# Performance work log

Measured on AMD Instinct MI355X. Metric: run time of the kernel, lower is better.

The kernel has to match this reference:

```python
import jax, jax.numpy as jnp
import numpy as np

NUM_HEADS = 32
HEAD_DIM = 512
EPS = 1e-12  # torch F.normalize eps


def setup_inputs() -> dict:
    key = jax.random.key(0)
    k1, k2, k3, k4, k5 = jax.random.split(key, 5)
    B, C, H, W = 32, 256, 64, 64
    return {
        "X": jax.random.normal(k1, (B, C, H, W), dtype=jnp.float32),
        "qkv_w": jax.random.normal(k2, (3 * HEAD_DIM, C), dtype=jnp.float32) * 0.02,
        "qkv_b": jax.random.normal(k3, (3 * HEAD_DIM,), dtype=jnp.float32) * 0.02,
        "proj_w": jax.random.normal(k4, (C, HEAD_DIM), dtype=jnp.float32) * 0.02,
        "proj_b": jax.random.normal(k5, (C,), dtype=jnp.float32) * 0.02,
    }


def _l2norm_axis1(x):
    # torch F.normalize(x, dim=1): x / max(||x||_2, eps)
    n = jnp.sqrt(jnp.sum(x * x, axis=1, keepdims=True))
    return x / jnp.maximum(n, EPS)


def reference(X, qkv_w, qkv_b, proj_w, proj_b):
    B, C, H, W = X.shape
    # 1x1 conv == channel matmul: [B,3*hd,H,W]
    qkv = jnp.einsum('bchw,oc->bohw', X, qkv_w) + qkv_b[None, :, None, None]
    # reshape to (B, 3, num_heads, head_dim, L) where L = H*W // num_heads
    qkv = qkv.reshape(B, 3, NUM_HEADS, HEAD_DIM, -1)
    q, k, v = qkv[:, 0], qkv[:, 1], qkv[:, 2]  # [B, nh, hd, L]
    # normalize across the num_heads axis (dim=1), as in the original code
    q = _l2norm_axis1(q)
    k = _l2norm_axis1(k)
    # attn = q^T @ k : [B, nh, L, L]
    attn = jnp.einsum('bhdl,bhdm->bhlm', q, k)
    attn = jax.nn.softmax(attn, axis=-1)
    # output = v @ attn^T : [B, nh, hd, L]
    out = jnp.einsum('bhdm,bhlm->bhdl', v, attn)
    out = out.reshape(B, HEAD_DIM, H, W)
    # proj 1x1 conv back to C channels
    out = jnp.einsum('bdhw,cd->bchw', out, proj_w) + proj_b[None, :, None, None]
    return out
```

## Files before the change

### kernel.cpp

```cpp
#include <hip/hip_runtime.h>
#include <stdint.h>


typedef float     f32x4   __attribute__((ext_vector_type(4)));
typedef short     bf16x8  __attribute__((ext_vector_type(8)));
typedef float     floatx4 __attribute__((ext_vector_type(4)));
typedef uint16_t  ushortx8 __attribute__((ext_vector_type(8)));
typedef uint16_t  ushortx4 __attribute__((ext_vector_type(4)));

#define DEVI static __device__ __forceinline__

DEVI float bf2f(uint16_t u) { union { uint32_t i; float f; } x; x.i = ((uint32_t)u) << 16; return x.f; }
DEVI uint16_t f2bf(float f) {
  union { float f; uint32_t i; } x; x.f = f;
  uint32_t r = x.i + 0x7fff + ((x.i >> 16) & 1);
  return (uint16_t)(r >> 16);
}

DEVI void gload16(const void* g, void* l) {
  __builtin_amdgcn_global_load_lds((const __attribute__((address_space(1))) void*)g,
                                   (__attribute__((address_space(3))) void*)l, 16, 0, 0);
}

DEVI float redmax16(float v) {
  v = fmaxf(v, __shfl_xor(v, 1)); v = fmaxf(v, __shfl_xor(v, 2));
  v = fmaxf(v, __shfl_xor(v, 4)); v = fmaxf(v, __shfl_xor(v, 8));
  return v;
}
DEVI float redsum16(float v) {
  v += __shfl_xor(v, 1); v += __shfl_xor(v, 2);
  v += __shfl_xor(v, 4); v += __shfl_xor(v, 8);
  return v;
}

__global__ __launch_bounds__(256) void k_transpose_x(const float* __restrict__ X,
                                                     uint16_t* __restrict__ Xt) {
  __shared__ float tile[64][65];
  int t = threadIdx.x;
  int st = blockIdx.x, ct = blockIdx.y, b = blockIdx.z;
  int row = t >> 2, cq = t & 3;
  const float* src = X + ((size_t)(b * 256 + ct * 64 + row)) * 4096 + st * 64 + cq * 16;
#pragma unroll
  for (int k = 0; k < 4; ++k) {
    floatx4 v = *(const floatx4*)(src + k * 4);
    tile[row][cq * 16 + k * 4 + 0] = v[0];
    tile[row][cq * 16 + k * 4 + 1] = v[1];
    tile[row][cq * 16 + k * 4 + 2] = v[2];
    tile[row][cq * 16 + k * 4 + 3] = v[3];
  }
  __syncthreads();
  int srow = t >> 2, oq = t & 3;
  ushortx8 o0, o1;
#pragma unroll
  for (int k = 0; k < 8; ++k) o0[k] = f2bf(tile[oq * 16 + k][srow]);
#pragma unroll
  for (int k = 0; k < 8; ++k) o1[k] = f2bf(tile[oq * 16 + 8 + k][srow]);
  uint16_t* dst = Xt + ((size_t)(b * 4096 + st * 64 + srow)) * 256 + ct * 64 + oq * 16;
  *(ushortx8*)dst = o0;
  *(ushortx8*)(dst + 8) = o1;
}

__global__ __launch_bounds__(256) void k_cvt_bf16(const float* __restrict__ src,
                                                  uint16_t* __restrict__ dst, int n) {
  int i = (blockIdx.x * 256 + threadIdx.x) * 4;
  if (i >= n) return;
  floatx4 v = *(const floatx4*)(src + i);
  ushortx4 o;
  o[0] = f2bf(v[0]); o[1] = f2bf(v[1]); o[2] = f2bf(v[2]); o[3] = f2bf(v[3]);
  *(ushortx4*)(dst + i) = o;
}

__global__ __launch_bounds__(256) void k_qkv_gemm(const uint16_t* __restrict__ W,
                                                  const uint16_t* __restrict__ Xt,
                                                  const float* __restrict__ bias_g,
                                                  uint16_t* __restrict__ qkv) {
  __shared__ __align__(16) union {
    uint16_t ab[2][128 * 64];
    uint16_t c[128 * 136];
  } sm;
  uint16_t* As = sm.ab[0];
  uint16_t* Bs = sm.ab[1];
  int t = threadIdx.x, lane = t & 63, wave = t >> 6;
  int ot = blockIdx.x, st = blockIdx.y, b = blockIdx.z;
  int wr = wave >> 1, wc = wave & 1;
  f32x4 acc[4][4] = {};
  int srow = lane >> 3;
  int sc_us = ((((lane & 7) * 16) ^ ((srow & 7) << 4)) >> 1);
  const uint16_t* Ag = W + (size_t)(ot * 128 + wave * 8 + srow) * 256;
  const uint16_t* Bg = Xt + ((size_t)(b * 4096 + st * 128 + wave * 8 + srow)) * 256;

  for (int kc = 0; kc < 4; ++kc) {
    __syncthreads();
#pragma unroll
    for (int c = 0; c < 4; ++c) {
      gload16(Ag + (size_t)(c * 32) * 256 + kc * 64 + sc_us, &As[(c * 32 + wave * 8) * 64]);
      gload16(Bg + (size_t)(c * 32) * 256 + kc * 64 + sc_us, &Bs[(c * 32 + wave * 8) * 64]);
    }
    __syncthreads();
#pragma unroll
    for (int kk = 0; kk < 2; ++kk) {
      bf16x8 a[4], bw[4];
#pragma unroll
      for (int i = 0; i < 4; ++i) {
        int r = wr * 64 + i * 16 + (lane & 15);
        a[i] = *(const bf16x8*)&As[r * 64 + ((kk * 32 + (lane >> 4) * 8) ^ ((r & 7) << 3))];
      }
#pragma unroll
      for (int j = 0; j < 4; ++j) {
        int r = wc * 64 + j * 16 + (lane & 15);
        bw[j] = *(const bf16x8*)&Bs[r * 64 + ((kk * 32 + (lane >> 4) * 8) ^ ((r & 7) << 3))];
      }
#pragma unroll
      for (int i = 0; i < 4; ++i)
#pragma unroll
        for (int j = 0; j < 4; ++j)
          acc[i][j] = __builtin_amdgcn_mfma_f32_16x16x32_bf16(a[i], bw[j], acc[i][j], 0, 0, 0);
    }
  }
  int o0 = ot * 128 + wr * 64;
  float bv[4][4];
#pragma unroll
  for (int i = 0; i < 4; ++i)
#pragma unroll
    for (int r = 0; r < 4; ++r) bv[i][r] = bias_g[o0 + i * 16 + (lane >> 4) * 4 + r];
  __syncthreads();
#pragma unroll
  for (int i = 0; i < 4; ++i)
#pragma unroll
    for (int j = 0; j < 4; ++j)
#pragma unroll
      for (int r = 0; r < 4; ++r) {
        int ol = wr * 64 + i * 16 + (lane >> 4) * 4 + r;
        int sl = wc * 64 + j * 16 + (lane & 15);
        sm.c[ol * 136 + sl] = f2bf(acc[i][j][r] + bv[i][r]);
      }
  __syncthreads();
  uint16_t* outb = qkv + ((size_t)b * 1536 + ot * 128) * 4096 + st * 128;
  int rrow = t >> 4, rcol = (t & 15) * 8;
#pragma unroll
  for (int p = 0; p < 8; ++p) {
    int row = p * 16 + rrow;
    ushortx8 v = *(ushortx8*)&sm.c[row * 136 + rcol];
    *(ushortx8*)(outb + (size_t)row * 4096 + rcol) = v;
  }
}

__global__ __launch_bounds__(256) void k_scales(const uint16_t* __restrict__ qkv,
                                                float* __restrict__ scaleB) {
  int t = threadIdx.x;
  int sc = blockIdx.x, g = blockIdx.y, b = blockIdx.z;
  const uint16_t* base = qkv + ((size_t)(b * 1536 + g * 512)) * 4096;
  float* sb = scaleB + (size_t)b * 524288 + (size_t)g * 65536;
  int c16 = t >> 4, so = t & 15;
  int s = sc * 128 + so * 8;
  float ss[8] = {};
  for (int h = 0; h < 32; ++h) {
    ushortx8 v = *(const ushortx8*)(base + ((size_t)(h * 16 + c16)) * 4096 + s);
#pragma unroll
    for (int j = 0; j < 8; ++j) { float f = bf2f(v[j]); ss[j] += f * f; }
  }
  floatx4 o0, o1;
#pragma unroll
  for (int j = 0; j < 4; ++j) o0[j] = 1.0f / fmaxf(sqrtf(ss[j]), 1e-12f);
#pragma unroll
  for (int j = 0; j < 4; ++j) o1[j] = 1.0f / fmaxf(sqrtf(ss[4 + j]), 1e-12f);
  *(floatx4*)(sb + c16 * 4096 + s) = o0;
  *(floatx4*)(sb + c16 * 4096 + s + 4) = o1;
}

__global__ __launch_bounds__(512, 4) void k_attn(const uint16_t* __restrict__ qkv,
                                                 const float* __restrict__ scaleB,
                                                 uint16_t* OtAll) {
  __shared__ __align__(16) uint16_t smemA[16384];
  __shared__ __align__(16) uint16_t Pb[16384];
  __shared__ float rsum[128];
  int t = threadIdx.x, lane = t & 63, w = t >> 6;
  int h = blockIdx.x, b = blockIdx.y;
  const uint16_t* qg = qkv + ((size_t)(b * 1536) + h * 16) * 4096;
  const uint16_t* kg = qkv + ((size_t)(b * 1536) + 512 + h * 16) * 4096;
  const float* sq = scaleB + (size_t)b * 524288;
  const float* sk = sq + 65536;
  uint16_t* QT = smemA;
  uint16_t* KT = smemA + 8192;

  int sl = t & 127;
  int dd8a = t >> 7;

  f32x4 accs[8] = {};
  for (int kc = 0; kc < 8; ++kc) {
    __syncthreads();
#pragma unroll
    for (int kq = 0; kq < 2; ++kq) {
      int dd8 = dd8a + kq * 4;
      int c16 = kc * 2 + (dd8 >> 2);
      int s0 = (dd8 & 3) * 8;
      const uint16_t* qrow = qg + (size_t)c16 * 4096 + sl;
      const uint16_t* krow = kg + (size_t)c16 * 4096 + sl;
      const float* sqr = sq + c16 * 4096 + sl;
      const float* skr = sk + c16 * 4096 + sl;
      ushortx8 oq, ok;
#pragma unroll
      for (int j = 0; j < 8; ++j) {
        int soff = (s0 + j) * 128;
        oq[j] = f2bf(bf2f(qrow[soff]) * sqr[soff]);
        ok[j] = f2bf(bf2f(krow[soff]) * skr[soff]);
      }
      int lidx = sl * 64 + ((dd8 * 8) ^ ((sl & 7) << 3));
      *(ushortx8*)&QT[lidx] = oq;
      *(ushortx8*)&KT[lidx] = ok;
    }
    __syncthreads();
#pragma unroll
    for (int kk = 0; kk < 2; ++kk) {
      int ra = w * 16 + (lane & 15);
      bf16x8 aq = *(const bf16x8*)&QT[ra * 64 + ((kk * 32 + (lane >> 4) * 8) ^ ((ra & 7) << 3))];
#pragma unroll
      for (int mf = 0; mf < 8; ++mf) {
        int rm = mf * 16 + (lane & 15);
        bf16x8 bk = *(const bf16x8*)&KT[rm * 64 + ((kk * 32 + (lane >> 4) * 8) ^ ((rm & 7) << 3))];
        accs[mf] = __builtin_amdgcn_mfma_f32_16x16x32_bf16(aq, bk, accs[mf], 0, 0, 0);
      }
    }
  }

#pragma unroll
  for (int r = 0; r < 4; ++r) {
    float mx = accs[0][r];
#pragma unroll
    for (int mf = 1; mf < 8; ++mf) mx = fmaxf(mx, accs[mf][r]);
    mx = redmax16(mx);
    float sum = 0.f;
#pragma unroll
    for (int mf = 0; mf < 8; ++mf) {
      float e = __expf(accs[mf][r] - mx);
      accs[mf][r] = e;
      sum += e;
    }
    sum = redsum16(sum);
    int l = w * 16 + (lane >> 4) * 4 + r;
    if ((lane & 15) == 0) rsum[l] = 1.0f / sum;
#pragma unroll
    for (int mf = 0; mf < 8; ++mf) {
      int m = mf * 16 + (lane & 15);
      Pb[l * 128 + (m ^ ((l & 7) << 3))] = f2bf(accs[mf][r]);
    }
  }
  __syncthreads();

  const uint16_t* vg = qkv + ((size_t)(b * 1536) + 1024 + h * 16) * 4096;
  uint16_t* OtT = OtAll + (size_t)b * 6291456;
  int vrow = lane >> 2;
  int vcol_us = ((((lane & 3) * 16) ^ ((vrow & 3) << 4)) >> 1);

#pragma unroll
  for (int lc = 0; lc < 2; ++lc) {
    f32x4 acco[4][4] = {};
    for (int mc = 0; mc < 4; ++mc) {
      __syncthreads();
#pragma unroll
      for (int c = 0; c < 4; ++c) {
        int d = w * 64 + c * 16 + vrow;
        gload16(vg + (size_t)(d >> 5) * 4096 + (d & 31) * 128 + mc * 32 + vcol_us,
                &smemA[(w * 64 + c * 16) * 32]);
      }
      __syncthreads();
      bf16x8 bp[4];
#pragma unroll
      for (int lf = 0; lf < 4; ++lf) {
        int l = lc * 64 + lf * 16 + (lane & 15);
        bp[lf] = *(const bf16x8*)&Pb[l * 128 + ((mc * 32 + (lane >> 4) * 8) ^ ((l & 7) << 3))];
      }
#pragma unroll
      for (int df = 0; df < 4; ++df) {
        int rv = w * 64 + df * 16 + (lane & 15);
        bf16x8 av = *(const bf16x8*)&smemA[rv * 32 + (((lane >> 4) * 8) ^ ((rv & 3) << 3))];
#pragma unroll
        for (int lf = 0; lf < 4; ++lf)
          acco[df][lf] = __builtin_amdgcn_mfma_f32_16x16x32_bf16(av, bp[lf], acco[df][lf], 0, 0, 0);
      }
    }
    float scl[4];
#pragma unroll
    for (int lf = 0; lf < 4; ++lf) scl[lf] = rsum[lc * 64 + lf * 16 + (lane & 15)];
#pragma unroll
    for (int df = 0; df < 4; ++df)
#pragma unroll
      for (int r = 0; r < 4; ++r) {
        int d = w * 64 + df * 16 + (lane >> 4) * 4 + r;
        uint16_t* orow = OtT + ((size_t)(h * 16 + (d >> 5))) * 4096 + (d & 31) * 128;
#pragma unroll
        for (int lf = 0; lf < 4; ++lf) {
          int l = lc * 64 + lf * 16 + (lane & 15);
          orow[l] = f2bf(acco[df][lf][r] * scl[lf]);
        }
      }
  }
}

__global__ __launch_bounds__(256) void k_proj_gemm(const uint16_t* __restrict__ Wp,
                                                   const uint16_t* __restrict__ OtAll,
                                                   const float* __restrict__ bias_g,
                                                   float* __restrict__ outp) {
  __shared__ __align__(16) uint16_t As[128 * 64];
  __shared__ __align__(16) uint16_t Bs[128 * 64];
  int t = threadIdx.x, lane = t & 63, wave = t >> 6;
  int st = blockIdx.x, ct = blockIdx.y, b = blockIdx.z;
  int wr = wave >> 1, wc = wave & 1;
  f32x4 acc[4][4] = {};
  int srow = lane >> 3;
  int sc_us = ((((lane & 7) * 16) ^ ((srow & 7) << 4)) >> 1);
  const uint16_t* Ag = Wp + (size_t)(ct * 128 + wave * 8 + srow) * 512;
  const uint16_t* Ob = OtAll + (size_t)b * 6291456;

  for (int kc = 0; kc < 8; ++kc) {
    __syncthreads();
#pragma unroll
    for (int c = 0; c < 4; ++c)
      gload16(Ag + (size_t)(c * 32) * 512 + kc * 64 + sc_us, &As[(c * 32 + wave * 8) * 64]);
#pragma unroll
    for (int k = 0; k < 4; ++k) {
      int cid = k * 256 + t;
      int row = cid & 127, dd8 = cid >> 7;
      const uint16_t* src = Ob + (size_t)(kc * 64 + dd8 * 8) * 4096 + st * 128 + row;
      ushortx8 o;
#pragma unroll
      for (int j = 0; j < 8; ++j) o[j] = src[(size_t)j * 4096];
      *(ushortx8*)&Bs[row * 64 + ((dd8 * 8) ^ ((row & 7) << 3))] = o;
    }
    __syncthreads();
#pragma unroll
    for (int kk = 0; kk < 2; ++kk) {
      bf16x8 a[4], bw[4];
#pragma unroll
      for (int i = 0; i < 4; ++i) {
        int r = wr * 64 + i * 16 + (lane & 15);
        a[i] = *(const bf16x8*)&As[r * 64 + ((kk * 32 + (lane >> 4) * 8) ^ ((r & 7) << 3))];
      }
#pragma unroll
      for (int j = 0; j < 4; ++j) {
        int r = wc * 64 + j * 16 + (lane & 15);
        bw[j] = *(const bf16x8*)&Bs[r * 64 + ((kk * 32 + (lane >> 4) * 8) ^ ((r & 7) << 3))];
      }
#pragma unroll
      for (int i = 0; i < 4; ++i)
#pragma unroll
        for (int j = 0; j < 4; ++j)
          acc[i][j] = __builtin_amdgcn_mfma_f32_16x16x32_bf16(a[i], bw[j], acc[i][j], 0, 0, 0);
    }
  }
  int c0 = ct * 128 + wr * 64, s0 = st * 128 + wc * 64;
  float bv[4][4];
#pragma unroll
  for (int i = 0; i < 4; ++i)
#pragma unroll
    for (int r = 0; r < 4; ++r) bv[i][r] = bias_g[c0 + i * 16 + (lane >> 4) * 4 + r];
#pragma unroll
  for (int i = 0; i < 4; ++i)
#pragma unroll
    for (int j = 0; j < 4; ++j)
#pragma unroll
      for (int r = 0; r < 4; ++r) {
        int c = c0 + i * 16 + (lane >> 4) * 4 + r;
        int s = s0 + j * 16 + (lane & 15);
        outp[((size_t)b * 256 + c) * 4096 + s] = acc[i][j][r] + bv[i][r];
      }
}

extern "C" void kernel_launch(void* const* d_in, const int* in_sizes, int n_in,
                              void* d_out, int out_size, void* d_ws, size_t ws_size,
                              hipStream_t stream) {
  const float* X      = (const float*)d_in[0];
  const float* qkv_w  = (const float*)d_in[1];
  const float* qkv_b  = (const float*)d_in[2];
  const float* proj_w = (const float*)d_in[3];
  const float* proj_b = (const float*)d_in[4];
  float* outp = (float*)d_out;

  const size_t SZ_XT  = 2097152;
  const size_t SZ_QKV = 12582912;
  const size_t SZ_W   = 786432 + 262144;

  int NB = 0;
  const int cand[6] = {32, 16, 8, 4, 2, 1};
  for (int ci = 0; ci < 6; ++ci) {
    size_t need = SZ_W + (size_t)cand[ci] * (SZ_XT + SZ_QKV);
    if (need <= ws_size) { NB = cand[ci]; break; }
  }
  if (NB == 0) return;

  char* ws = (char*)d_ws;
  uint16_t* Wqb  = (uint16_t*)(ws);
  uint16_t* Wpb  = (uint16_t*)(ws + 786432);
  char*     gbuf = ws + SZ_W;
  uint16_t* Xt   = (uint16_t*)(gbuf);
  uint16_t* qkvb = (uint16_t*)(gbuf + (size_t)NB * SZ_XT);
  float*    scaleB = (float*)Xt;

  k_cvt_bf16<<<dim3(384), 256, 0, stream>>>(qkv_w, Wqb, 1536 * 256);
  k_cvt_bf16<<<dim3(128), 256, 0, stream>>>(proj_w, Wpb, 256 * 512);

  for (int b0 = 0; b0 < 32; b0 += NB) {
    const float* Xg   = X + (size_t)b0 * 256 * 4096;
    float*       outg = outp + (size_t)b0 * 256 * 4096;
    k_transpose_x<<<dim3(64, 4, NB), 256, 0, stream>>>(Xg, Xt);
    k_qkv_gemm<<<dim3(12, 32, NB), 256, 0, stream>>>(Wqb, Xt, qkv_b, qkvb);
    k_scales<<<dim3(32, 2, NB), 256, 0, stream>>>(qkvb, scaleB);
    k_attn<<<dim3(32, NB), 512, 0, stream>>>(qkvb, scaleB, qkvb );
    k_proj_gemm<<<dim3(32, 2, NB), 256, 0, stream>>>(Wpb, qkvb , proj_b, outg);
  }
}
```

Before: 587.1 us.

## Shrink attention LDS footprint, split V staging, stage output stores through LDS

The attention kernel's shared staging buffer shrinks from 32KB to 20KB. Q/K are now staged one 16-row chunk per iteration in a padded layout (stride 40, no XOR swizzle), and V tiles are loaded in two halves into that same buffer. Output writes go through a per-wave padded LDS patch so each lane issues 16-byte global stores instead of scattered 2-byte stores. The aim is higher occupancy from the smaller LDS use and coalesced output writes. The cost is twice as many barriers in the QK loop and the V loop, plus extra LDS round trips on the output path.

```diff
diff --git a/kernel.cpp b/kernel.cpp
--- a/kernel.cpp
+++ b/kernel.cpp
@@ -131,8 +131,8 @@
 #pragma unroll
       for (int r = 0; r < 4; ++r) {
         int ol = wr * 64 + i * 16 + (lane >> 4) * 4 + r;
-        int sl = wc * 64 + j * 16 + (lane & 15);
-        sm.c[ol * 136 + sl] = f2bf(acc[i][j][r] + bv[i][r]);
+        int sl2 = wc * 64 + j * 16 + (lane & 15);
+        sm.c[ol * 136 + sl2] = f2bf(acc[i][j][r] + bv[i][r]);
       }
   __syncthreads();
   uint16_t* outb = qkv + ((size_t)b * 1536 + ot * 128) * 4096 + st * 128;
@@ -171,7 +171,7 @@
 __global__ __launch_bounds__(512, 4) void k_attn(const uint16_t* __restrict__ qkv,
                                                  const float* __restrict__ scaleB,
                                                  uint16_t* OtAll) {
-  __shared__ __align__(16) uint16_t smemA[16384];
+  __shared__ __align__(16) uint16_t stage[10240];
   __shared__ __align__(16) uint16_t Pb[16384];
   __shared__ float rsum[128];
   int t = threadIdx.x, lane = t & 63, w = t >> 6;
@@ -180,46 +180,37 @@
   const uint16_t* kg = qkv + ((size_t)(b * 1536) + 512 + h * 16) * 4096;
   const float* sq = scaleB + (size_t)b * 524288;
   const float* sk = sq + 65536;
-  uint16_t* QT = smemA;
-  uint16_t* KT = smemA + 8192;
+  uint16_t* QT = stage;
+  uint16_t* KT = stage + 5120;
 
   int sl = t & 127;
-  int dd8a = t >> 7;
+  int sb8 = t >> 7;
 
   f32x4 accs[8] = {};
-  for (int kc = 0; kc < 8; ++kc) {
-    __syncthreads();
-#pragma unroll
-    for (int kq = 0; kq < 2; ++kq) {
-      int dd8 = dd8a + kq * 4;
-      int c16 = kc * 2 + (dd8 >> 2);
-      int s0 = (dd8 & 3) * 8;
-      const uint16_t* qrow = qg + (size_t)c16 * 4096 + sl;
-      const uint16_t* krow = kg + (size_t)c16 * 4096 + sl;
-      const float* sqr = sq + c16 * 4096 + sl;
-      const float* skr = sk + c16 * 4096 + sl;
-      ushortx8 oq, ok;
-#pragma unroll
-      for (int j = 0; j < 8; ++j) {
-        int soff = (s0 + j) * 128;
-        oq[j] = f2bf(bf2f(qrow[soff]) * sqr[soff]);
-        ok[j] = f2bf(bf2f(krow[soff]) * skr[soff]);
-      }
-      int lidx = sl * 64 + ((dd8 * 8) ^ ((sl & 7) << 3));
-      *(ushortx8*)&QT[lidx] = oq;
-      *(ushortx8*)&KT[lidx] = ok;
-    }
-    __syncthreads();
-#pragma unroll
-    for (int kk = 0; kk < 2; ++kk) {
-      int ra = w * 16 + (lane & 15);
-      bf16x8 aq = *(const bf16x8*)&QT[ra * 64 + ((kk * 32 + (lane >> 4) * 8) ^ ((ra & 7) << 3))];
-#pragma unroll
-      for (int mf = 0; mf < 8; ++mf) {
-        int rm = mf * 16 + (lane & 15);
-        bf16x8 bk = *(const bf16x8*)&KT[rm * 64 + ((kk * 32 + (lane >> 4) * 8) ^ ((rm & 7) << 3))];
-        accs[mf] = __builtin_amdgcn_mfma_f32_16x16x32_bf16(aq, bk, accs[mf], 0, 0, 0);
-      }
+  for (int kc = 0; kc < 16; ++kc) {
+    const uint16_t* qrow = qg + (size_t)kc * 4096 + sl;
+    const uint16_t* krow = kg + (size_t)kc * 4096 + sl;
+    const float* sqr = sq + kc * 4096 + sl;
+    const float* skr = sk + kc * 4096 + sl;
+    ushortx8 oq, ok;
+#pragma unroll
+    for (int j = 0; j < 8; ++j) {
+      int soff = (sb8 * 8 + j) * 128;
+      oq[j] = f2bf(bf2f(qrow[soff]) * sqr[soff]);
+      ok[j] = f2bf(bf2f(krow[soff]) * skr[soff]);
+    }
+    __syncthreads();
+    int lidx = sl * 40 + sb8 * 8;
+    *(ushortx8*)&QT[lidx] = oq;
+    *(ushortx8*)&KT[lidx] = ok;
+    __syncthreads();
+    int ra = w * 16 + (lane & 15);
+    bf16x8 aq = *(const bf16x8*)&QT[ra * 40 + (lane >> 4) * 8];
+#pragma unroll
+    for (int mf = 0; mf < 8; ++mf) {
+      int rm = mf * 16 + (lane & 15);
+      bf16x8 bk = *(const bf16x8*)&KT[rm * 40 + (lane >> 4) * 8];
+      accs[mf] = __builtin_amdgcn_mfma_f32_16x16x32_bf16(aq, bk, accs[mf], 0, 0, 0);
     }
   }
 
@@ -249,21 +240,14 @@
 
   const uint16_t* vg = qkv + ((size_t)(b * 1536) + 1024 + h * 16) * 4096;
   uint16_t* OtT = OtAll + (size_t)b * 6291456;
+  uint16_t* Vt = stage;
   int vrow = lane >> 2;
   int vcol_us = ((((lane & 3) * 16) ^ ((vrow & 3) << 4)) >> 1);
 
 #pragma unroll
   for (int lc = 0; lc < 2; ++lc) {
-    f32x4 acco[4][4] = {};
+    f32x4 acco[2][2][4] = {};
     for (int mc = 0; mc < 4; ++mc) {
-      __syncthreads();
-#pragma unroll
-      for (int c = 0; c < 4; ++c) {
-        int d = w * 64 + c * 16 + vrow;
-        gload16(vg + (size_t)(d >> 5) * 4096 + (d & 31) * 128 + mc * 32 + vcol_us,
-                &smemA[(w * 64 + c * 16) * 32]);
-      }
-      __syncthreads();
       bf16x8 bp[4];
 #pragma unroll
       for (int lf = 0; lf < 4; ++lf) {
@@ -271,29 +255,58 @@
         bp[lf] = *(const bf16x8*)&Pb[l * 128 + ((mc * 32 + (lane >> 4) * 8) ^ ((l & 7) << 3))];
       }
 #pragma unroll
-      for (int df = 0; df < 4; ++df) {
-        int rv = w * 64 + df * 16 + (lane & 15);
-        bf16x8 av = *(const bf16x8*)&smemA[rv * 32 + (((lane >> 4) * 8) ^ ((rv & 3) << 3))];
-#pragma unroll
-        for (int lf = 0; lf < 4; ++lf)
-          acco[df][lf] = __builtin_amdgcn_mfma_f32_16x16x32_bf16(av, bp[lf], acco[df][lf], 0, 0, 0);
+      for (int half = 0; half < 2; ++half) {
+        __syncthreads();
+#pragma unroll
+        for (int c = 0; c < 2; ++c) {
+          int d = half * 256 + w * 32 + c * 16 + vrow;
+          gload16(vg + (size_t)(d >> 5) * 4096 + (d & 31) * 128 + mc * 32 + vcol_us,
+                  &Vt[(w * 32 + c * 16) * 32]);
+        }
+        __syncthreads();
+#pragma unroll
+        for (int df = 0; df < 2; ++df) {
+          int rv = w * 32 + df * 16 + (lane & 15);
+          bf16x8 av = *(const bf16x8*)&Vt[rv * 32 + (((lane >> 4) * 8) ^ ((rv & 3) << 3))];
+#pragma unroll
+          for (int lf = 0; lf < 4; ++lf)
+            acco[half][df][lf] =
+                __builtin_amdgcn_mfma_f32_16x16x32_bf16(av, bp[lf], acco[half][df][lf], 0, 0, 0);
+        }
       }
     }
     float scl[4];
 #pragma unroll
     for (int lf = 0; lf < 4; ++lf) scl[lf] = rsum[lc * 64 + lf * 16 + (lane & 15)];
-#pragma unroll
-    for (int df = 0; df < 4; ++df)
-#pragma unroll
-      for (int r = 0; r < 4; ++r) {
-        int d = w * 64 + df * 16 + (lane >> 4) * 4 + r;
-        uint16_t* orow = OtT + ((size_t)(h * 16 + (d >> 5))) * 4096 + (d & 31) * 128;
-#pragma unroll
-        for (int lf = 0; lf < 4; ++lf) {
-          int l = lc * 64 + lf * 16 + (lane & 15);
-          orow[l] = f2bf(acco[df][lf][r] * scl[lf]);
+
+    __syncthreads();
+    uint16_t* patch = stage + w * 1056;
+#pragma unroll
+    for (int half = 0; half < 2; ++half) {
+      uint16_t* obase = OtT + (size_t)(h * 16 + half * 8 + w) * 4096;
+#pragma unroll
+      for (int df = 0; df < 2; ++df) {
+#pragma unroll
+        for (int r = 0; r < 4; ++r) {
+          int dlocal = (lane >> 4) * 4 + r;
+#pragma unroll
+          for (int lf = 0; lf < 4; ++lf)
+            patch[dlocal * 66 + lf * 16 + (lane & 15)] = f2bf(acco[half][df][lf][r] * scl[lf]);
         }
-      }
+        asm volatile("s_waitcnt lgkmcnt(0)" ::: "memory");
+        __builtin_amdgcn_sched_barrier(0);
+        int dl = lane >> 2, l8 = (lane & 3) * 16;
+        uint16_t tmp[16];
+#pragma unroll
+        for (int e = 0; e < 8; ++e)
+          *(uint32_t*)&tmp[e * 2] = *(const uint32_t*)&patch[dl * 66 + l8 + e * 2];
+        uint16_t* gp = obase + (df * 16 + dl) * 128 + lc * 64 + l8;
+        *(ushortx8*)gp = *(ushortx8*)&tmp[0];
+        *(ushortx8*)(gp + 8) = *(ushortx8*)&tmp[8];
+        asm volatile("s_waitcnt lgkmcnt(0)" ::: "memory");
+        __builtin_amdgcn_sched_barrier(0);
+      }
+    }
   }
 }
 
```

Result: no change. 578.3 us (-1.5%).
